# Performance work log

Hardware: AMD Instinct MI355X
Metric: run time of the kernel (lower is better)

## Reference

```python
import jax, jax.numpy as jnp
import numpy as np

NUM_HEADS = 16
HEAD_DIM = 64
HIDDEN = NUM_HEADS * HEAD_DIM  # 1024
B, T = 32, 512


def setup_inputs() -> dict:
    key = jax.random.key(0)
    ks = jax.random.split(key, 10)
    s = 1.0 / np.sqrt(HIDDEN)
    inp = {
        "x": jax.random.normal(ks[0], (B, HIDDEN, T), dtype=jnp.float32),
        "mask": jax.random.randint(ks[1], (B, T), 0, 2, dtype=jnp.int32),
        "Wq": jax.random.uniform(ks[2], (HIDDEN, HIDDEN), jnp.float32, -s, s),
        "bq": jax.random.uniform(ks[3], (HIDDEN,), jnp.float32, -s, s),
        "Wk": jax.random.uniform(ks[4], (HIDDEN, HIDDEN), jnp.float32, -s, s),
        "bk": jax.random.uniform(ks[5], (HIDDEN,), jnp.float32, -s, s),
        "Wv": jax.random.uniform(ks[6], (HIDDEN, HIDDEN), jnp.float32, -s, s),
        "bv": jax.random.uniform(ks[7], (HIDDEN,), jnp.float32, -s, s),
        "Wo": jax.random.uniform(ks[8], (HIDDEN, HIDDEN), jnp.float32, -s, s),
        "bo": jax.random.uniform(ks[9], (HIDDEN,), jnp.float32, -s, s),
    }
    return inp


def reference(x, mask, Wq, bq, Wk, bk, Wv, bv, Wo, bo):
    # x: [B, hidden, T] -> tokens along last axis
    b, h, t = x.shape
    xt = jnp.swapaxes(x, 1, 2)  # [B, T, hidden]

    def heads(w, bias):
        y = xt @ w.T + bias                       # [B, T, hidden]
        return y.reshape(b, t, NUM_HEADS, HEAD_DIM).transpose(0, 2, 1, 3)  # [B, nh, T, hd]

    q = heads(Wq, bq)
    k = heads(Wk, bk)
    v = heads(Wv, bv)

    scores = jnp.einsum("bhqd,bhkd->bhqk", q, k) / jnp.sqrt(jnp.float32(HEAD_DIM))
    # masked_fill(mask==0, -inf) then clamp to [-50, 50]: masked entries become -50
    scores = jnp.where(mask[:, None, None, :] == 0, -jnp.inf, scores)
    scores = jnp.clip(scores, -50.0, 50.0)
    attn = jax.nn.softmax(scores, axis=-1)        # [B, nh, T, T]
    out = jnp.einsum("bhqk,bhkd->bhqd", attn, v)  # [B, nh, T, hd]
    out = out.transpose(0, 2, 1, 3).reshape(b, t, h)
    out = out @ Wo.T + bo                         # [B, T, hidden]
    return out.max(axis=1)                        # [B, hidden]
```

## Files before the change

### kernel.cpp

```cpp
#include <hip/hip_runtime.h>


typedef _Float16 half8 __attribute__((ext_vector_type(8)));
typedef _Float16 half4 __attribute__((ext_vector_type(4)));
typedef float floatx4 __attribute__((ext_vector_type(4)));
typedef unsigned uintx2 __attribute__((ext_vector_type(2)));

#define HID 1024
#define TT 512
#define NB 32
#define QSCALE 0.1803368801111244f
#define SB2 72.13475204444817f

__device__ __forceinline__ void gload16(const void* g, void* l) {
    __builtin_amdgcn_global_load_lds(
        (const __attribute__((address_space(1))) unsigned int*)g,
        (__attribute__((address_space(3))) unsigned int*)l, 16, 0, 0);
}

__device__ __forceinline__ unsigned fkey(float f) {
    unsigned u = __float_as_uint(f);
    return (u & 0x80000000u) ? ~u : (u | 0x80000000u);
}
__device__ __forceinline__ float funkey(unsigned k) {
    unsigned u = (k & 0x80000000u) ? (k ^ 0x80000000u) : ~k;
    return __uint_as_float(u);
}

__global__ __launch_bounds__(256) void prep_kernel(
    const float* __restrict__ Wq, const float* __restrict__ Wk,
    const float* __restrict__ Wv, const float* __restrict__ Wo,
    _Float16* __restrict__ Wcat,
    const float* __restrict__ x, _Float16* __restrict__ xT,
    unsigned* __restrict__ omax,
    const float* __restrict__ bq, float* __restrict__ bqs)
{
    __shared__ float tile[64][65];
    const int bid = blockIdx.x;
    if (bid < 4096) {
        int i4 = bid * 256 + threadIdx.x;
        int sec = i4 >> 18;
        int off4 = i4 & ((1 << 18) - 1);
        const float* src = (sec == 0) ? Wq : (sec == 1) ? Wk
                          : (sec == 2) ? Wv : Wo;
        float4 v = ((const float4*)src)[off4];
        if (sec == 0) {
            v.x *= QSCALE; v.y *= QSCALE; v.z *= QSCALE; v.w *= QSCALE;
        }
        half4 h = {(_Float16)v.x, (_Float16)v.y, (_Float16)v.z, (_Float16)v.w};
        *(half4*)(Wcat + (size_t)i4 * 4) = h;
    } else if (bid < 8192) {
        int idx = bid - 4096;
        int b = idx >> 7, h0 = ((idx >> 3) & 15) * 64, t0 = (idx & 7) * 64;
        int tx = threadIdx.x & 15, ty = threadIdx.x >> 4;
        const float* xb = x + ((size_t)b * HID + h0) * TT + t0;
        for (int p = 0; p < 4; p++) {
            int r = ty + 16 * p;
            float4 v = *(const float4*)(xb + (size_t)r * TT + tx * 4);
            tile[r][tx * 4 + 0] = v.x;
            tile[r][tx * 4 + 1] = v.y;
            tile[r][tx * 4 + 2] = v.z;
            tile[r][tx * 4 + 3] = v.w;
        }
        __syncthreads();
        int hc = (threadIdx.x & 7) * 8, tb = threadIdx.x >> 3;
        for (int rd = 0; rd < 2; rd++) {
            int tt = tb + 32 * rd;
            half8 pk;
            for (int k = 0; k < 8; k++)
                pk[k] = (_Float16)tile[hc + k][tt];
            *(half8*)(xT + ((size_t)b * TT + t0 + tt) * HID + h0 + hc) = pk;
        }
    } else if (bid < 8320) {
        omax[(bid - 8192) * 256 + threadIdx.x] = 0u;
    } else {
        int i = (bid - 8320) * 256 + threadIdx.x;
        bqs[i] = bq[i] * QSCALE;
    }
}

__device__ __forceinline__ void gemm_mainloop(
    const _Float16* __restrict__ Arows,
    const _Float16* __restrict__ Brows,
    _Float16* aT, _Float16* bT, floatx4 acc[4][4], int tid)
{
    const int lane = tid & 63, wid = tid >> 6;
    const int l15 = lane & 15, quad = lane >> 4;
    const int wm = (wid >> 1) * 64, wn = (wid & 1) * 64;

    const int srow = lane >> 3;
    const int sg = (lane & 7) ^ srow;
    const _Float16* ga = Arows + (size_t)(wid * 32 + srow) * 1024 + sg * 8;
    const _Float16* gb = Brows + (size_t)(wid * 32 + srow) * 1024 + sg * 8;
    _Float16* la = aT + wid * 32 * 64;
    _Float16* lb = bT + wid * 32 * 64;

    const int pa = quad ^ (l15 & 7);

    for (int k0 = 0; k0 < 1024; k0 += 64) {
        for (int p = 0; p < 4; p++) {
            gload16(ga + k0 + p * 8 * 1024, la + p * 8 * 64);
            gload16(gb + k0 + p * 8 * 1024, lb + p * 8 * 64);
        }
        __syncthreads();
        for (int kk = 0; kk < 2; kk++) {
            const int pg = kk ? (pa ^ 4) : pa;
            half8 af[4], bf[4];
            for (int mi = 0; mi < 4; mi++)
                af[mi] = *(half8*)(aT + (wm + mi * 16 + l15) * 64 + pg * 8);
            for (int ni = 0; ni < 4; ni++)
                bf[ni] = *(half8*)(bT + (wn + ni * 16 + l15) * 64 + pg * 8);
            for (int mi = 0; mi < 4; mi++)
                for (int ni = 0; ni < 4; ni++)
                    acc[mi][ni] = __builtin_amdgcn_mfma_f32_16x16x32_f16(
                        af[mi], bf[ni], acc[mi][ni], 0, 0, 0);
        }
        __syncthreads();
    }
}

__global__ __launch_bounds__(256) void gemm1_kernel(
    const _Float16* __restrict__ Wcat,
    const float* __restrict__ bqs, const float* __restrict__ bk,
    const float* __restrict__ bv,
    const _Float16* __restrict__ xT,
    _Float16* __restrict__ QT, _Float16* __restrict__ KT,
    _Float16* __restrict__ Vb)
{
    __shared__ __align__(16) char smem[34816];
    _Float16* aT = (_Float16*)smem;
    _Float16* bTl = aT + 128 * 64;

    const int tid = threadIdx.x;
    const int id = blockIdx.x;
    const int xcd = id & 7, slot = id >> 3;
    const int grp = xcd + 8 * (slot / 24);
    const int m0 = (slot % 24) * 128;
    const int n0 = (grp & 3) * 128;
    const int b = grp >> 2;
    const int lane = tid & 63, wid = tid >> 6;
    const int l15 = lane & 15, quad = lane >> 4;
    const int wm = (wid >> 1) * 64, wn = (wid & 1) * 64;

    floatx4 acc[4][4] = {};
    gemm_mainloop(Wcat + (size_t)m0 * 1024,
                  xT + ((size_t)b * TT + n0) * HID,
                  aT, bTl, acc, tid);

    const int sec = m0 >> 10;
    const int mo = m0 & 1023;

    if (sec < 2) {
        const float* bias = (sec == 0) ? bqs : bk;
        _Float16* dst = (sec == 0) ? QT : KT;
        _Float16* tr = (_Float16*)smem;
        for (int mi = 0; mi < 4; mi++) {
            float bs[4];
            for (int r = 0; r < 4; r++)
                bs[r] = bias[mo + wm + mi * 16 + quad * 4 + r];
            for (int ni = 0; ni < 4; ni++) {
                half4 pk;
                for (int r = 0; r < 4; r++)
                    pk[r] = (_Float16)(acc[mi][ni][r] + bs[r]);
                int tl = wn + ni * 16 + l15;
                int ol = wm + mi * 16 + quad * 4;
                *(half4*)(tr + tl * 136 + ol) = pk;
            }
        }
        __syncthreads();
        int tl = tid >> 1, cb = (tid & 1) * 64;
        for (int ch = 0; ch < 8; ch++) {
            uint4 v = *(uint4*)(tr + tl * 136 + cb + ch * 8);
            *(uint4*)(dst + ((size_t)b * TT + n0 + tl) * HID + mo + cb + ch * 8) = v;
        }
    } else {
        for (int mi = 0; mi < 4; mi++) {
            float bs[4];
            for (int r = 0; r < 4; r++)
                bs[r] = bv[mo + wm + mi * 16 + quad * 4 + r];
            for (int ni = 0; ni < 4; ni++) {
                int t = n0 + wn + ni * 16 + l15;
                for (int r = 0; r < 4; r++) {
                    int o = mo + wm + mi * 16 + quad * 4 + r;
                    Vb[((size_t)b * HID + o) * TT + t] =
                        (_Float16)(acc[mi][ni][r] + bs[r]);
                }
            }
        }
    }
}

__global__ __launch_bounds__(256) void attn_kernel(
    const _Float16* __restrict__ QT, const _Float16* __restrict__ KT,
    const _Float16* __restrict__ Vb, const int* __restrict__ mask,
    _Float16* __restrict__ OcT)
{
    __shared__ __align__(16) _Float16 kvbuf[4 * 4096];
    __shared__ __align__(16) _Float16 ps[2 * 4096];
    __shared__ __align__(16) float msf[2][64];

    const int id = blockIdx.x;
    const int xcd = id & 7, slot = id >> 3;
    const int grp = xcd + 8 * (slot >> 2);
    const int q0 = (slot & 3) * 128;
    const int hd = grp & 15, b = grp >> 4;
    const int tid = threadIdx.x;
    const int lane = tid & 63, wid = tid >> 6;
    const int l15 = lane & 15, quad = lane >> 4;

    const _Float16* QTb = QT + ((size_t)b * TT + q0) * HID + hd * 64;
    const _Float16* KTb = KT + (size_t)b * TT * HID + hd * 64;
    const _Float16* Vbb = Vb + ((size_t)b * HID + hd * 64) * TT;
    const int* mb = mask + b * TT;

    const int srow = lane >> 3;
    const int sg = (lane & 7) ^ srow;
    const int pa = quad ^ (l15 & 7);
    const int pz = l15 & 7;

    for (int qt = 0; qt < 2; qt++)
        for (int p = 0; p < 2; p++) {
            int r = p * 32 + wid * 8 + srow;
            gload16(QTb + (size_t)(qt * 64 + r) * HID + sg * 8,
                    kvbuf + qt * 4096 + (p * 32 + wid * 8) * 64);
        }
    __syncthreads();
    half8 bq[2][2];
    for (int qt = 0; qt < 2; qt++) {
        bq[qt][0] = *(half8*)(kvbuf + qt * 4096 + (wid * 16 + l15) * 64 + pa * 8);
        bq[qt][1] = *(half8*)(kvbuf + qt * 4096 + (wid * 16 + l15) * 64 + (pa ^ 4) * 8);
    }
    __syncthreads();

    auto stage = [&](int jcn, int bufn) {
        int t0n = jcn * 64;
        _Float16* kd = kvbuf + bufn * 4096;
        _Float16* vd = kvbuf + (2 + bufn) * 4096;
        for (int p = 0; p < 2; p++) {
            int r = p * 32 + wid * 8 + srow;
            gload16(KTb + (size_t)(t0n + r) * HID + sg * 8,
                    kd + (p * 32 + wid * 8) * 64);
            gload16(Vbb + (size_t)r * TT + t0n + sg * 8,
                    vd + (p * 32 + wid * 8) * 64);
        }
        if (tid < 64) msf[bufn][tid] = mb[t0n + tid] ? SB2 : -SB2;
    };

    stage(0, 0);

    floatx4 oacc[2][4] = {};
    float rs[2] = {0.f, 0.f};
    const float lo = -SB2;

    for (int jc = 0; jc < 8; jc++) {
        const int cur = jc & 1;
        __syncthreads();
        if (jc < 7) stage(jc + 1, 1 - cur);

        const _Float16* ks = kvbuf + cur * 4096;
        const _Float16* vs = kvbuf + (2 + cur) * 4096;

        for (int jt = 0; jt < 4; jt++) {
            half8 ka0 = *(half8*)(ks + (jt * 16 + l15) * 64 + pa * 8);
            half8 ka1 = *(half8*)(ks + (jt * 16 + l15) * 64 + (pa ^ 4) * 8);
            floatx4 hi = *(floatx4*)(&msf[cur][jt * 16 + quad * 4]);
            for (int qt = 0; qt < 2; qt++) {
                floatx4 sc = {0.f, 0.f, 0.f, 0.f};
                sc = __builtin_amdgcn_mfma_f32_16x16x32_f16(ka0, bq[qt][0], sc, 0, 0, 0);
                sc = __builtin_amdgcn_mfma_f32_16x16x32_f16(ka1, bq[qt][1], sc, 0, 0, 0);
                float e0 = __builtin_amdgcn_exp2f(fminf(fmaxf(sc[0], lo), hi[0]));
                float e1 = __builtin_amdgcn_exp2f(fminf(fmaxf(sc[1], lo), hi[1]));
                float e2 = __builtin_amdgcn_exp2f(fminf(fmaxf(sc[2], lo), hi[2]));
                float e3 = __builtin_amdgcn_exp2f(fminf(fmaxf(sc[3], lo), hi[3]));
                rs[qt] += (e0 + e1) + (e2 + e3);
                unsigned uA = __builtin_bit_cast(
                    unsigned, __builtin_amdgcn_cvt_pkrtz(e0, e1));
                unsigned uB = __builtin_bit_cast(
                    unsigned, __builtin_amdgcn_cvt_pkrtz(e2, e3));
                uintx2 uv = {uA, uB};
                half4 pk = __builtin_bit_cast(half4, uv);
                int g = jt * 2 + (quad >> 1);
                *(half4*)(ps + qt * 4096 + (wid * 16 + l15) * 64 + (g ^ pz) * 8 +
                          (quad & 1) * 4) = pk;
            }
        }
        for (int kc = 0; kc < 2; kc++) {
            int g = kc * 4 + quad;
            half8 bv8[4];
            for (int d4 = 0; d4 < 4; d4++)
                bv8[d4] = *(half8*)(vs + (d4 * 16 + l15) * 64 + (g ^ pz) * 8);
            for (int qt = 0; qt < 2; qt++) {
                half8 ap = *(half8*)(ps + qt * 4096 + (wid * 16 + l15) * 64 +
                                     (g ^ pz) * 8);
                for (int d4 = 0; d4 < 4; d4++)
                    oacc[qt][d4] = __builtin_amdgcn_mfma_f32_16x16x32_f16(
                        ap, bv8[d4], oacc[qt][d4], 0, 0, 0);
            }
        }
    }

    for (int qt = 0; qt < 2; qt++) {
        float s = rs[qt];
        s += __shfl_xor(s, 16, 64);
        s += __shfl_xor(s, 32, 64);
        s = 1.0f / s;
        float inv[4];
        for (int r = 0; r < 4; r++) inv[r] = __shfl(s, quad * 4 + r, 64);
        for (int d4 = 0; d4 < 4; d4++)
            for (int r = 0; r < 4; r++) {
                int t = q0 + qt * 64 + wid * 16 + quad * 4 + r;
                int c = hd * 64 + d4 * 16 + l15;
                OcT[((size_t)b * TT + t) * HID + c] =
                    (_Float16)(oacc[qt][d4][r] * inv[r]);
            }
    }
}

__global__ __launch_bounds__(256) void gemm2_kernel(
    const _Float16* __restrict__ Wo16, const _Float16* __restrict__ OcT,
    unsigned* __restrict__ omax)
{
    __shared__ __align__(16) char smem[2 * 128 * 64 * 2];
    _Float16* aT = (_Float16*)smem;
    _Float16* bTl = aT + 128 * 64;

    const int tid = threadIdx.x;
    const int id = blockIdx.x;
    const int xcd = id & 7, slot = id >> 3;
    const int grp = xcd + 8 * (slot >> 3);
    const int m0 = (slot & 7) * 128;
    const int n0 = (grp & 3) * 128;
    const int b = grp >> 2;
    const int lane = tid & 63, wid = tid >> 6;
    const int l15 = lane & 15, quad = lane >> 4;
    const int wm = (wid >> 1) * 64;

    floatx4 acc[4][4] = {};
    gemm_mainloop(Wo16 + (size_t)m0 * 1024,
                  OcT + ((size_t)b * TT + n0) * HID,
                  aT, bTl, acc, tid);

    for (int mi = 0; mi < 4; mi++)
        for (int r = 0; r < 4; r++) {
            float v = acc[mi][0][r];
            for (int ni = 1; ni < 4; ni++) v = fmaxf(v, acc[mi][ni][r]);
            for (int d = 1; d < 16; d <<= 1) v = fmaxf(v, __shfl_xor(v, d, 64));
            if (l15 == 0) {
                int o = m0 + wm + mi * 16 + quad * 4 + r;
                atomicMax(&omax[b * HID + o], fkey(v));
            }
        }
}

__global__ __launch_bounds__(256) void final_kernel(
    const unsigned* __restrict__ omax, const float* __restrict__ bo,
    float* __restrict__ out)
{
    int i = blockIdx.x * 256 + threadIdx.x;
    out[i] = funkey(omax[i]) + bo[i & 1023];
}

extern "C" void kernel_launch(void* const* d_in, const int* in_sizes, int n_in,
                              void* d_out, int out_size, void* d_ws, size_t ws_size,
                              hipStream_t stream)
{
    const float* x  = (const float*)d_in[0];
    const int* mask = (const int*)d_in[1];
    const float* Wq = (const float*)d_in[2];
    const float* bq = (const float*)d_in[3];
    const float* Wk = (const float*)d_in[4];
    const float* bk = (const float*)d_in[5];
    const float* Wv = (const float*)d_in[6];
    const float* bv = (const float*)d_in[7];
    const float* Wo = (const float*)d_in[8];
    const float* bo = (const float*)d_in[9];
    float* out = (float*)d_out;

    char* ws = (char*)d_ws;
    _Float16* Wcat = (_Float16*)(ws);
    _Float16* xT   = (_Float16*)(ws + (8ull  << 20));
    _Float16* QT   = (_Float16*)(ws + (40ull << 20));
    _Float16* KT   = (_Float16*)(ws + (72ull << 20));
    _Float16* Vb   = (_Float16*)(ws + (104ull << 20));
    _Float16* OcT  = (_Float16*)(ws + (136ull << 20));
    unsigned* omax = (unsigned*)(ws + (168ull << 20));
    float*    bqs  = (float*)(ws + (168ull << 20) + (128ull << 10));

    prep_kernel<<<8324, 256, 0, stream>>>(Wq, Wk, Wv, Wo, Wcat, x, xT, omax,
                                          bq, bqs);
    gemm1_kernel<<<3072, 256, 0, stream>>>(Wcat, bqs, bk, bv, xT, QT, KT, Vb);
    attn_kernel<<<2048, 256, 0, stream>>>(QT, KT, Vb, mask, OcT);
    gemm2_kernel<<<1024, 256, 0, stream>>>(Wcat + (3ull << 20), OcT, omax);
    final_kernel<<<128, 256, 0, stream>>>(omax, bo, out);
}
```

Measured before the change: 349.2 us.

## Replace GEMM mainloop with 256x256 tiles and ping-pong double-buffered LDS pipeline

Both projection GEMMs move from 128x128 tiles with 256 threads to 256x256 tiles with 512 threads (8 waves). Operands are double-buffered in LDS through async global-to-LDS loads. The loads are interleaved with MFMA quadrants using explicit vmcnt waits, barriers and setprio, so memory traffic overlaps compute. This aims to raise arithmetic intensity and hide load latency, at the cost of 128KB of LDS per block, fewer blocks, and a two-pass epilogue for the transposed Q/K stores.

```diff
diff --git a/kernel.cpp b/kernel.cpp
--- a/kernel.cpp
+++ b/kernel.cpp
@@ -79,47 +79,130 @@
     }
 }
 
-__device__ __forceinline__ void gemm_mainloop(
-    const _Float16* __restrict__ Arows,
-    const _Float16* __restrict__ Brows,
-    _Float16* aT, _Float16* bT, floatx4 acc[4][4], int tid)
-{
-    const int lane = tid & 63, wid = tid >> 6;
+
+#define PH_PRE do { \
+    __builtin_amdgcn_s_barrier(); \
+    asm volatile("s_waitcnt lgkmcnt(0)" ::: "memory"); \
+    __builtin_amdgcn_sched_barrier(0); \
+    __builtin_amdgcn_s_setprio(1); \
+} while (0)
+
+#define PH_POST(N) do { \
+    __builtin_amdgcn_s_setprio(0); \
+    asm volatile("s_waitcnt vmcnt(" #N ")" ::: "memory"); \
+    __builtin_amdgcn_s_barrier(); \
+} while (0)
+
+#define LDA(P, MH) do { \
+    const _Float16* ab_ = lds + (P) * 16384 + (MH) * 8192 + aoff; \
+    af[0][0] = *(const half8*)(ab_ + pb0); \
+    af[0][1] = *(const half8*)(ab_ + pb1); \
+    af[1][0] = *(const half8*)(ab_ + 1024 + pb0); \
+    af[1][1] = *(const half8*)(ab_ + 1024 + pb1); \
+    af[2][0] = *(const half8*)(ab_ + 2048 + pb0); \
+    af[2][1] = *(const half8*)(ab_ + 2048 + pb1); \
+    af[3][0] = *(const half8*)(ab_ + 3072 + pb0); \
+    af[3][1] = *(const half8*)(ab_ + 3072 + pb1); \
+} while (0)
+
+#define LDB(P, NH) do { \
+    const _Float16* bb_ = lds + 32768 + (P) * 16384 + (NH) * 8192 + boff; \
+    bf[NH][0][0] = *(const half8*)(bb_ + pb0); \
+    bf[NH][0][1] = *(const half8*)(bb_ + pb1); \
+    bf[NH][1][0] = *(const half8*)(bb_ + 1024 + pb0); \
+    bf[NH][1][1] = *(const half8*)(bb_ + 1024 + pb1); \
+} while (0)
+
+#define STAGE_A(P, MH, K0) do { \
+    _Float16* d_ = lds + (P) * 16384 + (MH) * 8192 + wst; \
+    gload16(ag + (MH) * 64 * 1024 + (K0), d_); \
+    gload16(ag + (128 + (MH) * 64) * 1024 + (K0), d_ + 4096); \
+} while (0)
+
+#define STAGE_B(P, NH, K0) do { \
+    _Float16* d_ = lds + 32768 + (P) * 16384 + (NH) * 8192 + wst; \
+    gload16(bg + (NH) * 32 * 1024 + (K0), d_); \
+    gload16(bg + (128 + (NH) * 32) * 1024 + (K0), d_ + 4096); \
+} while (0)
+
+#define MFMAQ(MH, NH) do { \
+    _Pragma("unroll") \
+    for (int j_ = 0; j_ < 4; ++j_) { \
+        _Pragma("unroll") \
+        for (int n_ = 0; n_ < 2; ++n_) { \
+            floatx4 c_ = acc[(MH) * 4 + j_][(NH) * 2 + n_]; \
+            c_ = __builtin_amdgcn_mfma_f32_16x16x32_f16( \
+                af[j_][0], bf[NH][n_][0], c_, 0, 0, 0); \
+            c_ = __builtin_amdgcn_mfma_f32_16x16x32_f16( \
+                af[j_][1], bf[NH][n_][1], c_, 0, 0, 0); \
+            acc[(MH) * 4 + j_][(NH) * 2 + n_] = c_; \
+        } \
+    } \
+} while (0)
+
+__device__ __forceinline__ void mainloop256(
+    const _Float16* __restrict__ Ag,
+    const _Float16* __restrict__ Bg,
+    _Float16* lds, floatx4 acc[8][4], int tid)
+{
+    const int lane = tid & 63;
+    const int w = tid >> 6, wr = w >> 2, wc = w & 3;
     const int l15 = lane & 15, quad = lane >> 4;
-    const int wm = (wid >> 1) * 64, wn = (wid & 1) * 64;
-
-    const int srow = lane >> 3;
-    const int sg = (lane & 7) ^ srow;
-    const _Float16* ga = Arows + (size_t)(wid * 32 + srow) * 1024 + sg * 8;
-    const _Float16* gb = Brows + (size_t)(wid * 32 + srow) * 1024 + sg * 8;
-    _Float16* la = aT + wid * 32 * 64;
-    _Float16* lb = bT + wid * 32 * 64;
-
     const int pa = quad ^ (l15 & 7);
-
-    for (int k0 = 0; k0 < 1024; k0 += 64) {
-        for (int p = 0; p < 4; p++) {
-            gload16(ga + k0 + p * 8 * 1024, la + p * 8 * 64);
-            gload16(gb + k0 + p * 8 * 1024, lb + p * 8 * 64);
-        }
-        __syncthreads();
-        for (int kk = 0; kk < 2; kk++) {
-            const int pg = kk ? (pa ^ 4) : pa;
-            half8 af[4], bf[4];
-            for (int mi = 0; mi < 4; mi++)
-                af[mi] = *(half8*)(aT + (wm + mi * 16 + l15) * 64 + pg * 8);
-            for (int ni = 0; ni < 4; ni++)
-                bf[ni] = *(half8*)(bT + (wn + ni * 16 + l15) * 64 + pg * 8);
-            for (int mi = 0; mi < 4; mi++)
-                for (int ni = 0; ni < 4; ni++)
-                    acc[mi][ni] = __builtin_amdgcn_mfma_f32_16x16x32_f16(
-                        af[mi], bf[ni], acc[mi][ni], 0, 0, 0);
-        }
-        __syncthreads();
-    }
-}
-
-__global__ __launch_bounds__(256) void gemm1_kernel(
+    const int pb0 = pa * 8, pb1 = (pa ^ 4) * 8;
+    const int aoff = (wr * 64 + l15) * 64;
+    const int boff = (wc * 32 + l15) * 64;
+    const int wst = w * 512;
+    const int r = tid >> 3;
+    const int sg = (tid & 7) ^ (r & 7);
+    const int nbase = ((r >> 5) << 6) + (r & 31);
+    const _Float16* ag = Ag + (size_t)r * 1024 + sg * 8;
+    const _Float16* bg = Bg + (size_t)nbase * 1024 + sg * 8;
+
+    half8 af[4][2], bf[2][2][2];
+
+    STAGE_A(0, 0, 0); STAGE_B(0, 0, 0); STAGE_B(0, 1, 0); STAGE_A(0, 1, 0);
+    STAGE_A(1, 0, 64); STAGE_B(1, 0, 64); STAGE_B(1, 1, 64);
+    asm volatile("s_waitcnt vmcnt(10)" ::: "memory");
+    __builtin_amdgcn_s_barrier();
+
+    for (int i = 0; i < 7; ++i) {
+        const int kb = i * 128 + 64;
+        const int kn0 = kb + 64, kn1 = kb + 128;
+        LDA(0, 0); LDB(0, 0); STAGE_A(1, 1, kb);
+        PH_PRE; MFMAQ(0, 0); PH_POST(10);
+        LDB(0, 1);            STAGE_A(0, 0, kn0);
+        PH_PRE; MFMAQ(0, 1); PH_POST(10);
+        LDA(0, 1);            STAGE_B(0, 0, kn0);
+        PH_PRE; MFMAQ(1, 1); PH_POST(10);
+                              STAGE_B(0, 1, kn0);
+        PH_PRE; MFMAQ(1, 0); PH_POST(10);
+        LDA(1, 0); LDB(1, 0); STAGE_A(0, 1, kn0);
+        PH_PRE; MFMAQ(0, 0); PH_POST(10);
+        LDB(1, 1);            STAGE_A(1, 0, kn1);
+        PH_PRE; MFMAQ(0, 1); PH_POST(10);
+        LDA(1, 1);            STAGE_B(1, 0, kn1);
+        PH_PRE; MFMAQ(1, 1); PH_POST(10);
+                              STAGE_B(1, 1, kn1);
+        PH_PRE; MFMAQ(1, 0); PH_POST(10);
+    }
+    LDA(0, 0); LDB(0, 0); STAGE_A(1, 1, 960);
+    PH_PRE; MFMAQ(0, 0); PH_POST(10);
+    LDB(0, 1);
+    PH_PRE; MFMAQ(0, 1); PH_POST(8);
+    LDA(0, 1);
+    PH_PRE; MFMAQ(1, 1); PH_POST(6);
+    PH_PRE; MFMAQ(1, 0); PH_POST(4);
+    LDA(1, 0); LDB(1, 0);
+    PH_PRE; MFMAQ(0, 0); PH_POST(2);
+    LDB(1, 1);
+    PH_PRE; MFMAQ(0, 1); PH_POST(0);
+    LDA(1, 1);
+    PH_PRE; MFMAQ(1, 1); MFMAQ(1, 0);
+    __builtin_amdgcn_s_setprio(0);
+}
+
+__global__ __launch_bounds__(512, 2) void gemm1_kernel(
     const _Float16* __restrict__ Wcat,
     const float* __restrict__ bqs, const float* __restrict__ bk,
     const float* __restrict__ bv,
@@ -127,25 +210,22 @@
     _Float16* __restrict__ QT, _Float16* __restrict__ KT,
     _Float16* __restrict__ Vb)
 {
-    __shared__ __align__(16) char smem[34816];
-    _Float16* aT = (_Float16*)smem;
-    _Float16* bTl = aT + 128 * 64;
-
+    __shared__ __align__(16) _Float16 smem[65536];
     const int tid = threadIdx.x;
     const int id = blockIdx.x;
     const int xcd = id & 7, slot = id >> 3;
-    const int grp = xcd + 8 * (slot / 24);
-    const int m0 = (slot % 24) * 128;
-    const int n0 = (grp & 3) * 128;
-    const int b = grp >> 2;
-    const int lane = tid & 63, wid = tid >> 6;
+    const int grp = xcd + 8 * (slot / 12);
+    const int m0 = (slot % 12) * 256;
+    const int n0 = (grp & 1) * 256;
+    const int bb = grp >> 1;
+    const int lane = tid & 63;
+    const int w = tid >> 6, wr = w >> 2, wc = w & 3;
     const int l15 = lane & 15, quad = lane >> 4;
-    const int wm = (wid >> 1) * 64, wn = (wid & 1) * 64;
-
-    floatx4 acc[4][4] = {};
-    gemm_mainloop(Wcat + (size_t)m0 * 1024,
-                  xT + ((size_t)b * TT + n0) * HID,
-                  aT, bTl, acc, tid);
+
+    floatx4 acc[8][4] = {};
+    mainloop256(Wcat + (size_t)m0 * 1024,
+                xT + ((size_t)bb * TT + n0) * HID, smem, acc, tid);
+    __syncthreads();
 
     const int sec = m0 >> 10;
     const int mo = m0 & 1023;
@@ -153,37 +233,42 @@
     if (sec < 2) {
         const float* bias = (sec == 0) ? bqs : bk;
         _Float16* dst = (sec == 0) ? QT : KT;
-        _Float16* tr = (_Float16*)smem;
-        for (int mi = 0; mi < 4; mi++) {
+        _Float16* tr = smem;
+        for (int h = 0; h < 2; ++h) {
+            if (wr == h) {
+                for (int mi = 0; mi < 8; ++mi) {
+                    float bs[4];
+                    for (int rr = 0; rr < 4; ++rr)
+                        bs[rr] = bias[mo + h * 128 + mi * 16 + quad * 4 + rr];
+                    for (int ni = 0; ni < 4; ++ni) {
+                        half4 pk;
+                        for (int rr = 0; rr < 4; ++rr)
+                            pk[rr] = (_Float16)(acc[mi][ni][rr] + bs[rr]);
+                        *(half4*)(tr + (wc * 64 + ni * 16 + l15) * 136 +
+                                  mi * 16 + quad * 4) = pk;
+                    }
+                }
+            }
+            __syncthreads();
+            const int row = tid >> 4, off = (tid & 15) * 8;
+            for (int s = 0; s < 8; ++s) {
+                uint4 v = *(uint4*)(tr + (row + 32 * s) * 136 + off);
+                *(uint4*)(dst + ((size_t)bb * TT + n0 + row + 32 * s) * HID +
+                          mo + h * 128 + off) = v;
+            }
+            __syncthreads();
+        }
+    } else {
+        for (int mi = 0; mi < 8; ++mi) {
             float bs[4];
-            for (int r = 0; r < 4; r++)
-                bs[r] = bias[mo + wm + mi * 16 + quad * 4 + r];
-            for (int ni = 0; ni < 4; ni++) {
-                half4 pk;
-                for (int r = 0; r < 4; r++)
-                    pk[r] = (_Float16)(acc[mi][ni][r] + bs[r]);
-                int tl = wn + ni * 16 + l15;
-                int ol = wm + mi * 16 + quad * 4;
-                *(half4*)(tr + tl * 136 + ol) = pk;
-            }
-        }
-        __syncthreads();
-        int tl = tid >> 1, cb = (tid & 1) * 64;
-        for (int ch = 0; ch < 8; ch++) {
-            uint4 v = *(uint4*)(tr + tl * 136 + cb + ch * 8);
-            *(uint4*)(dst + ((size_t)b * TT + n0 + tl) * HID + mo + cb + ch * 8) = v;
-        }
-    } else {
-        for (int mi = 0; mi < 4; mi++) {
-            float bs[4];
-            for (int r = 0; r < 4; r++)
-                bs[r] = bv[mo + wm + mi * 16 + quad * 4 + r];
-            for (int ni = 0; ni < 4; ni++) {
-                int t = n0 + wn + ni * 16 + l15;
-                for (int r = 0; r < 4; r++) {
-                    int o = mo + wm + mi * 16 + quad * 4 + r;
-                    Vb[((size_t)b * HID + o) * TT + t] =
-                        (_Float16)(acc[mi][ni][r] + bs[r]);
+            for (int rr = 0; rr < 4; ++rr)
+                bs[rr] = bv[mo + wr * 128 + mi * 16 + quad * 4 + rr];
+            for (int ni = 0; ni < 4; ++ni) {
+                int t = n0 + wc * 64 + ni * 16 + l15;
+                for (int rr = 0; rr < 4; ++rr) {
+                    int o = mo + wr * 128 + mi * 16 + quad * 4 + rr;
+                    Vb[((size_t)bb * HID + o) * TT + t] =
+                        (_Float16)(acc[mi][ni][rr] + bs[rr]);
                 }
             }
         }
@@ -316,38 +401,37 @@
     }
 }
 
-__global__ __launch_bounds__(256) void gemm2_kernel(
+__global__ __launch_bounds__(512, 2) void gemm2_kernel(
     const _Float16* __restrict__ Wo16, const _Float16* __restrict__ OcT,
     unsigned* __restrict__ omax)
 {
-    __shared__ __align__(16) char smem[2 * 128 * 64 * 2];
-    _Float16* aT = (_Float16*)smem;
-    _Float16* bTl = aT + 128 * 64;
-
+    __shared__ __align__(16) _Float16 smem[65536];
     const int tid = threadIdx.x;
     const int id = blockIdx.x;
     const int xcd = id & 7, slot = id >> 3;
-    const int grp = xcd + 8 * (slot >> 3);
-    const int m0 = (slot & 7) * 128;
-    const int n0 = (grp & 3) * 128;
-    const int b = grp >> 2;
-    const int lane = tid & 63, wid = tid >> 6;
+    const int grp = xcd + 8 * (slot >> 2);
+    const int m0 = (slot & 3) * 256;
+    const int n0 = (grp & 1) * 256;
+    const int bb = grp >> 1;
+    const int lane = tid & 63;
+    const int w = tid >> 6, wr = w >> 2;
     const int l15 = lane & 15, quad = lane >> 4;
-    const int wm = (wid >> 1) * 64;
-
-    floatx4 acc[4][4] = {};
-    gemm_mainloop(Wo16 + (size_t)m0 * 1024,
-                  OcT + ((size_t)b * TT + n0) * HID,
-                  aT, bTl, acc, tid);
-
-    for (int mi = 0; mi < 4; mi++)
-        for (int r = 0; r < 4; r++) {
-            float v = acc[mi][0][r];
-            for (int ni = 1; ni < 4; ni++) v = fmaxf(v, acc[mi][ni][r]);
-            for (int d = 1; d < 16; d <<= 1) v = fmaxf(v, __shfl_xor(v, d, 64));
+
+    floatx4 acc[8][4] = {};
+    mainloop256(Wo16 + (size_t)m0 * 1024,
+                OcT + ((size_t)bb * TT + n0) * HID, smem, acc, tid);
+
+    for (int mi = 0; mi < 8; ++mi)
+        for (int rr = 0; rr < 4; ++rr) {
+            float v = acc[mi][0][rr];
+            v = fmaxf(v, acc[mi][1][rr]);
+            v = fmaxf(v, acc[mi][2][rr]);
+            v = fmaxf(v, acc[mi][3][rr]);
+            for (int d = 1; d < 16; d <<= 1)
+                v = fmaxf(v, __shfl_xor(v, d, 64));
             if (l15 == 0) {
-                int o = m0 + wm + mi * 16 + quad * 4 + r;
-                atomicMax(&omax[b * HID + o], fkey(v));
+                int o = m0 + wr * 128 + mi * 16 + quad * 4 + rr;
+                atomicMax(&omax[bb * HID + o], fkey(v));
             }
         }
 }
@@ -388,8 +472,8 @@
 
     prep_kernel<<<8324, 256, 0, stream>>>(Wq, Wk, Wv, Wo, Wcat, x, xT, omax,
                                           bq, bqs);
-    gemm1_kernel<<<3072, 256, 0, stream>>>(Wcat, bqs, bk, bv, xT, QT, KT, Vb);
+    gemm1_kernel<<<768, 512, 0, stream>>>(Wcat, bqs, bk, bv, xT, QT, KT, Vb);
     attn_kernel<<<2048, 256, 0, stream>>>(QT, KT, Vb, mask, OcT);
-    gemm2_kernel<<<1024, 256, 0, stream>>>(Wcat + (3ull << 20), OcT, omax);
+    gemm2_kernel<<<256, 512, 0, stream>>>(Wcat + (3ull << 20), OcT, omax);
     final_kernel<<<128, 256, 0, stream>>>(omax, bo, out);
 }
```

After: 325.0 us. 6.9% less time.
